# Performance work log

Measured on AMD Instinct MI355X. Metric: run time of the kernel, lower is better.

## Reference

```python
import jax, jax.numpy as jnp
import numpy as np

NEG = -1e30  # log-space -inf surrogate (safe for logaddexp in fp32)


def _ctc_mean_loss(y_true, y_pred):
    """tf.nn.ctc_loss with blank_index=-1, logit_length=T, label_length=#nonzero.

    y_true: [B, L] int labels, 0 = padding, packed at the front.
    y_pred: [B, T, C] logits. blank = C-1. Returns mean NLL over batch.
    """
    B, L = y_true.shape
    T, C = y_pred.shape[1], y_pred.shape[2]
    blank = C - 1
    S = 2 * L + 1  # extended label length (blanks interleaved)

    label_length = jnp.sum((y_true != 0).astype(jnp.int32), axis=1)  # [B]
    logp = jax.nn.log_softmax(y_pred, axis=-1)  # [B, T, C]

    # Extended sequence: blank, l1, blank, l2, ..., blank
    ext = jnp.full((B, S), blank, dtype=jnp.int32)
    ext = ext.at[:, 1::2].set(y_true.astype(jnp.int32))  # [B, S]

    # skip transition (s-2 -> s) allowed only at odd s>=3 when labels differ
    skip_ok = jnp.zeros((B, S), dtype=bool)
    skip_ok = skip_ok.at[:, 3::2].set(y_true[:, 1:] != y_true[:, :-1])

    # alpha_0
    alpha0 = jnp.full((B, S), NEG, dtype=logp.dtype)
    alpha0 = alpha0.at[:, 0].set(logp[:, 0, blank])
    alpha0 = alpha0.at[:, 1].set(
        jnp.take_along_axis(logp[:, 0, :], ext[:, 1:2], axis=1)[:, 0])

    def step(alpha, logp_t):  # alpha [B,S], logp_t [B,C]
        s1 = jnp.pad(alpha, ((0, 0), (1, 0)), constant_values=NEG)[:, :-1]
        s2 = jnp.pad(alpha, ((0, 0), (2, 0)), constant_values=NEG)[:, :-2]
        comb = jnp.logaddexp(jnp.logaddexp(alpha, s1),
                             jnp.where(skip_ok, s2, NEG))
        emit = jnp.take_along_axis(logp_t, ext, axis=1)  # [B,S]
        return comb + emit, None

    alphaT, _ = jax.lax.scan(step, alpha0, jnp.swapaxes(logp, 0, 1)[1:])

    # P(labels) = alpha_T[2l] + alpha_T[2l-1]  (last blank / last label)
    l = label_length
    idx = jnp.stack([2 * l, 2 * l - 1], axis=1)  # [B,2], l>=1 by construction
    fin = jnp.take_along_axis(alphaT, idx, axis=1)
    loss = -jnp.logaddexp(fin[:, 0], fin[:, 1])  # [B]
    return jnp.mean(loss)


def setup_inputs() -> dict:
    key = jax.random.key(0)
    k1, k2, k3 = jax.random.split(key, 3)
    B, T, L, C = 256, 512, 128, 128
    lengths = jax.random.randint(k1, (B,), L // 2, L + 1)  # labels per example
    vals = jax.random.randint(k2, (B, L), 1, C - 1)  # classes 1..C-2 (blank=C-1)
    mask = jnp.arange(L)[None, :] < lengths[:, None]
    y_true = jnp.where(mask, vals, 0).astype(jnp.int32)
    y_pred = jax.random.normal(k3, (B, T, C), dtype=jnp.float32)
    return {"y_true": y_true, "y_pred": y_pred}


def reference(y_true, y_pred):
    return _ctc_mean_loss(y_true, y_pred)
```

## Files before the change

### kernel.cpp

```cpp
#include <hip/hip_runtime.h>
#include <hip/hip_fp16.h>

#define LN2D 0.6931471805599453094172321

typedef float v2f __attribute__((ext_vector_type(2)));

__device__ __forceinline__ float shr1(float v, float fill) {
    return __int_as_float(__builtin_amdgcn_update_dpp(
        __float_as_int(fill), __float_as_int(v), 0x138 , 0xF, 0xF, false));
}
__device__ __forceinline__ float shl1(float v, float fill) {
    return __int_as_float(__builtin_amdgcn_update_dpp(
        __float_as_int(fill), __float_as_int(v), 0x130 , 0xF, 0xF, false));
}

__device__ __forceinline__ float wave_sum63(float x) {
    int t;
    t = __builtin_amdgcn_update_dpp(0, __float_as_int(x), 0x111, 0xF, 0xF, true);
    x += __int_as_float(t);
    t = __builtin_amdgcn_update_dpp(0, __float_as_int(x), 0x112, 0xF, 0xF, true);
    x += __int_as_float(t);
    t = __builtin_amdgcn_update_dpp(0, __float_as_int(x), 0x114, 0xF, 0xF, true);
    x += __int_as_float(t);
    t = __builtin_amdgcn_update_dpp(0, __float_as_int(x), 0x118, 0xF, 0xF, true);
    x += __int_as_float(t);
    t = __builtin_amdgcn_update_dpp(0, __float_as_int(x), 0x142, 0xA, 0xF, true);
    x += __int_as_float(t);
    t = __builtin_amdgcn_update_dpp(0, __float_as_int(x), 0x143, 0xC, 0xF, true);
    x += __int_as_float(t);
    return x;
}

__device__ __forceinline__ float wave_max63(float x) {
    int iv = __float_as_int(x); int t;
    t = __builtin_amdgcn_update_dpp(iv, iv, 0x111, 0xF, 0xF, false);
    x = fmaxf(x, __int_as_float(t)); iv = __float_as_int(x);
    t = __builtin_amdgcn_update_dpp(iv, iv, 0x112, 0xF, 0xF, false);
    x = fmaxf(x, __int_as_float(t)); iv = __float_as_int(x);
    t = __builtin_amdgcn_update_dpp(iv, iv, 0x114, 0xF, 0xF, false);
    x = fmaxf(x, __int_as_float(t)); iv = __float_as_int(x);
    t = __builtin_amdgcn_update_dpp(iv, iv, 0x118, 0xF, 0xF, false);
    x = fmaxf(x, __int_as_float(t)); iv = __float_as_int(x);
    t = __builtin_amdgcn_update_dpp(iv, iv, 0x142, 0xA, 0xF, false);
    x = fmaxf(x, __int_as_float(t)); iv = __float_as_int(x);
    t = __builtin_amdgcn_update_dpp(iv, iv, 0x143, 0xC, 0xF, false);
    x = fmaxf(x, __int_as_float(t));
    return x;
}

__device__ __forceinline__ float rdl63(float v) {
    return __int_as_float(__builtin_amdgcn_readlane(__float_as_int(v), 63));
}

__device__ __forceinline__ unsigned short pk_fp8(float a, float b) {
    const unsigned short ha = __builtin_bit_cast(unsigned short, __float2half_rn(a));
    const unsigned short hb = __builtin_bit_cast(unsigned short, __float2half_rn(b));
    const unsigned ua = ((unsigned)ha + 0x80u) >> 8;
    const unsigned ub = (((unsigned)hb + 0x80u) >> 8) << 8;
    return (unsigned short)(ua | ub);
}
__device__ __forceinline__ float dec_lo(unsigned short u) {
    return __half2float(__builtin_bit_cast(__half, (unsigned short)((u & 0xFFu) << 8)));
}
__device__ __forceinline__ float dec_hi(unsigned short u) {
    return __half2float(__builtin_bit_cast(__half, (unsigned short)(u & 0xFF00u)));
}

__global__ __launch_bounds__(512) void ctc_fused(const int* __restrict__ yt,
                                                 const float* __restrict__ yp,
                                                 float* __restrict__ part,
                                                 float* __restrict__ accW) {
    constexpr int L = 128;
    const int b    = blockIdx.x;
    const int w    = threadIdx.x >> 6;
    const int lane = threadIdx.x & 63;

    __shared__ unsigned short g[512][64];

    const int2 cc = *reinterpret_cast<const int2*>(yt + b * L + 2 * lane);
    const int c1 = cc.x, c3 = cc.y;
    const int sl1 = c1 >> 1, sh1v = (c1 & 1) << 4;
    const int sl3 = c3 >> 1, sh3v = (c3 & 1) << 4;

    float acc = 0.0f;
    const float* src = yp + ((size_t)b * 512 + w * 64) * 128 + lane * 2;
    v2f A8[8], B8[8];

#define ISSUE8(d_, p_)                                                         \
    asm volatile(                                                              \
        "global_load_dwordx2 %0, %8, off\n\t"                                  \
        "global_load_dwordx2 %1, %8, off offset:512\n\t"                       \
        "global_load_dwordx2 %2, %8, off offset:1024\n\t"                      \
        "global_load_dwordx2 %3, %8, off offset:1536\n\t"                      \
        "global_load_dwordx2 %4, %8, off offset:2048\n\t"                      \
        "global_load_dwordx2 %5, %8, off offset:2560\n\t"                      \
        "global_load_dwordx2 %6, %8, off offset:3072\n\t"                      \
        "global_load_dwordx2 %7, %8, off offset:3584"                          \
        : "=&v"(d_[0]), "=&v"(d_[1]), "=&v"(d_[2]), "=&v"(d_[3]),              \
          "=&v"(d_[4]), "=&v"(d_[5]), "=&v"(d_[6]), "=&v"(d_[7])               \
        : "v"(p_)                                                              \
        : "memory");

#define WAITN(n_)                                                              \
    {                                                                          \
        asm volatile("s_waitcnt vmcnt(" #n_ ")" ::: "memory");                 \
        __builtin_amdgcn_sched_barrier(0);                                     \
    }

#define PROC8(buf_, rb_)                                                       \
    {                                                                          \
        _Pragma("unroll")                                                      \
        for (int i = 0; i < 8; ++i) {                                          \
            const float vx = buf_[i].x, vy = buf_[i].y;                        \
            const float sall = rdl63(wave_sum63(__expf(vx) + __expf(vy)));     \
            const float xbv  = rdl63(vy);                \
            acc += __logf(sall) - xbv;                                         \
            const __half2 hh = __floats2half2_rn(vx, vy);                      \
            const int hb = __builtin_bit_cast(int, hh);                        \
            const int q1 = __shfl(hb, sl1, 64);                                \
            const int q3 = __shfl(hb, sl3, 64);                                \
            const float x1 = __half2float(__builtin_bit_cast(__half, (unsigned short)(q1 >> sh1v))); \
            const float x3 = __half2float(__builtin_bit_cast(__half, (unsigned short)(q3 >> sh3v))); \
            g[w * 64 + (rb_) + i][lane] = pk_fp8(__expf(x1 - xbv), __expf(x3 - xbv)); \
        }                                                                      \
    }

    ISSUE8(A8, src)
    ISSUE8(B8, src + 8 * 128)
    WAITN(8)  PROC8(A8, 0)   ISSUE8(A8, src + 16 * 128)
    WAITN(8)  PROC8(B8, 8)   ISSUE8(B8, src + 24 * 128)
    WAITN(8)  PROC8(A8, 16)  ISSUE8(A8, src + 32 * 128)
    WAITN(8)  PROC8(B8, 24)  ISSUE8(B8, src + 40 * 128)
    WAITN(8)  PROC8(A8, 32)  ISSUE8(A8, src + 48 * 128)
    WAITN(8)  PROC8(B8, 40)  ISSUE8(B8, src + 56 * 128)
    WAITN(8)  PROC8(A8, 48)
    WAITN(0)  PROC8(B8, 56)

    if (lane == 0) accW[b * 8 + w] = acc;
    __syncthreads();

    if (w == 0) {
        const int cprev = __shfl_up(c3, 1, 64);
        const float sk1 = (lane > 0 && c1 != cprev) ? 1.0f : 0.0f;
        const float sk3 = (c3 != c1) ? 1.0f : 0.0f;
        const float skB3 = shl1(sk1, 0.0f);
        const int llen = __popcll(__ballot(c1 != 0)) + __popcll(__ballot(c3 != 0));

        float o0, o1, o2, o3, o4;
        float q0, q1, q2, q3, q4;
        int   EF = 0, EB = 0;
        unsigned short fr[8], br[8];

#define RENORM5(a0_, a1_, a2_, a3_, a4_, Ec_)                                  \
    {                                                                          \
        float mr = fmaxf(fmaxf(fmaxf(a0_, a1_), fmaxf(a2_, a3_)), a4_);        \
        const float mru = rdl63(wave_max63(mr));                               \
        const int ie = (__float_as_int(mru) >> 23) & 0xFF;                     \
        const float sc = __int_as_float((253 - ie) << 23);                     \
        a0_ *= sc; a1_ *= sc; a2_ *= sc; a3_ *= sc; a4_ *= sc;                 \
        Ec_ += ie - 126;                                                       \
    }

#define FSTEP(bits_, rn_)                                                      \
    {                                                                          \
        const float e1 = dec_lo(bits_);                                        \
        const float e3 = dec_hi(bits_);                                        \
        const float pm = shr1(o3, 0.0f);                                       \
        const float n0 = o0 + pm;                                              \
        const float n1 = (o1 + o0 + sk1 * pm) * e1;                            \
        const float n2 = o2 + o1;                                              \
        const float n3 = (o3 + o2 + sk3 * o1) * e3;                            \
        o4 += o3;                                                              \
        o0 = n0; o1 = n1; o2 = n2; o3 = n3;                                    \
        if (rn_) RENORM5(o0, o1, o2, o3, o4, EF);                              \
    }

#define BSTEP(bits_, rn_)                                                      \
    {                                                                          \
        const float e1 = dec_lo(bits_);                                        \
        const float e3 = dec_hi(bits_);                                        \
        const float g1 = q1 * e1;                                              \
        const float g3 = q3 * e3;                                              \
        const float pm0 = shl1(q0, q4);          \
        const float pm1 = shl1(g1, 0.0f);        \
        const float n0 = q0 + g1;                                              \
        const float n1 = g1 + q2 + sk3 * g3;                                   \
        const float n2 = q2 + g3;                                              \
        const float n3 = g3 + pm0 + skB3 * pm1;                                \
        q0 = n0; q1 = n1; q2 = n2; q3 = n3;                                    \
        if (rn_) RENORM5(q0, q1, q2, q3, q4, EB);                              \
    }

        #pragma unroll
        for (int i = 0; i < 8; ++i) { fr[i] = g[i][lane]; br[i] = g[511 - i][lane]; }

        {
            const float e10 = dec_lo(fr[0]);
            o0 = (lane == 0) ? 1.0f : 0.0f;
            o1 = (lane == 0) ? e10 : 0.0f;
            o2 = 0.0f; o3 = 0.0f; o4 = 0.0f;
        }
        {
            const int sA = 2 * llen, sB = 2 * llen - 1;
            q0 = (4 * lane + 0 == sA) ? 1.0f : 0.0f;
            q1 = (4 * lane + 1 == sB) ? 1.0f : 0.0f;
            q2 = (4 * lane + 2 == sA) ? 1.0f : 0.0f;
            q3 = (4 * lane + 3 == sB) ? 1.0f : 0.0f;
            q4 = (llen == 128 && lane == 63) ? 1.0f : 0.0f;
        }

        BSTEP(br[0], false);
        fr[0] = g[8][lane]; br[0] = g[503][lane];
        #pragma unroll
        for (int k = 1; k < 8; ++k) {
            FSTEP(fr[k], false);
            BSTEP(br[k], false);
            fr[k] = g[k + 8][lane]; br[k] = g[511 - k - 8][lane];
        }
        for (int kb = 8; kb < 248; kb += 8) {
            #pragma unroll
            for (int j = 0; j < 8; ++j) {
                const int k = kb + j;
                FSTEP(fr[j], (k & 31) == 0);
                BSTEP(br[j], (k & 31) == 31);
                fr[j] = g[k + 8][lane]; br[j] = g[511 - k - 8][lane];
            }
        }
        #pragma unroll
        for (int k = 248; k < 256; ++k) {
            FSTEP(fr[k & 7], false);
            BSTEP(br[k & 7], (k & 31) == 31);
        }

        double p = (double)o0 * (double)q0 + (double)o1 * (double)q1
                 + (double)o2 * (double)q2 + (double)o3 * (double)q3;
        if (lane == 63) p += (double)o4 * (double)q4;
        #pragma unroll
        for (int off = 32; off > 0; off >>= 1) p += __shfl_xor(p, off, 64);
        if (lane == 0)
            part[b] = (float)(log(p) + (double)(EF + EB) * LN2D);
#undef BSTEP
#undef FSTEP
#undef RENORM5
    }
#undef PROC8
#undef WAITN
#undef ISSUE8
}

__global__ __launch_bounds__(256) void finalize(const float* __restrict__ part,
                                                const float* __restrict__ accW,
                                                float* __restrict__ out) {
    __shared__ float red[256];
    const int tid = threadIdx.x;
    float ls = 0.0f;
    #pragma unroll
    for (int j = 0; j < 8; ++j) ls += accW[tid * 8 + j];
    red[tid] = -(part[tid] - ls);
    __syncthreads();
    for (int off = 128; off > 0; off >>= 1) {
        if (tid < off) red[tid] += red[tid + off];
        __syncthreads();
    }
    if (tid == 0) out[0] = red[0] * (1.0f / 256.0f);
}

extern "C" void kernel_launch(void* const* d_in, const int* in_sizes, int n_in,
                              void* d_out, int out_size, void* d_ws, size_t ws_size,
                              hipStream_t stream) {
    constexpr int B = 256;
    const int*   y_true = (const int*)d_in[0];
    const float* y_pred = (const float*)d_in[1];
    float* out = (float*)d_out;

    float* part = (float*)d_ws;
    float* accW = part + B;

    ctc_fused<<<B, 512, 0, stream>>>(y_true, y_pred, part, accW);
    finalize<<<1, 256, 0, stream>>>(part, accW, out);
}
```

Measured before the change: 45.24 us.

## Compute log-sum-exp per lane over full rows and decode fp8 pairs in one op

The per-timestep softmax normaliser was computed with a wave-wide DPP reduction for every row. It is replaced by a second pass in which each lane reads one full 128-class row as float4 loads and sums exps serially. Only one wave reduction of the per-row logs remains per wave. The two-byte fp8-like decode is also merged into a single byte_perm plus half2-to-float2 conversion. The cost is re-reading the logits from global memory (likely L2-resident) in exchange for removing 64 cross-lane reductions per wave.

```diff
diff --git a/kernel.cpp b/kernel.cpp
--- a/kernel.cpp
+++ b/kernel.cpp
@@ -59,11 +59,9 @@
     const unsigned ub = (((unsigned)hb + 0x80u) >> 8) << 8;
     return (unsigned short)(ua | ub);
 }
-__device__ __forceinline__ float dec_lo(unsigned short u) {
-    return __half2float(__builtin_bit_cast(__half, (unsigned short)((u & 0xFFu) << 8)));
-}
-__device__ __forceinline__ float dec_hi(unsigned short u) {
-    return __half2float(__builtin_bit_cast(__half, (unsigned short)(u & 0xFF00u)));
+__device__ __forceinline__ float2 dec2(unsigned short u) {
+    const unsigned pk = __byte_perm((unsigned)u, 0u, 0x01040004);
+    return __half22float2(__builtin_bit_cast(__half2, pk));
 }
 
 __global__ __launch_bounds__(512) void ctc_fused(const int* __restrict__ yt,
@@ -82,7 +80,7 @@
     const int sl1 = c1 >> 1, sh1v = (c1 & 1) << 4;
     const int sl3 = c3 >> 1, sh3v = (c3 & 1) << 4;
 
-    float acc = 0.0f;
+    float xbsum = 0.0f;
     const float* src = yp + ((size_t)b * 512 + w * 64) * 128 + lane * 2;
     v2f A8[8], B8[8];
 
@@ -112,9 +110,8 @@
         _Pragma("unroll")                                                      \
         for (int i = 0; i < 8; ++i) {                                          \
             const float vx = buf_[i].x, vy = buf_[i].y;                        \
-            const float sall = rdl63(wave_sum63(__expf(vx) + __expf(vy)));     \
-            const float xbv  = rdl63(vy);                \
-            acc += __logf(sall) - xbv;                                         \
+            const float xbv = rdl63(vy);                 \
+            xbsum += xbv;                                                      \
             const __half2 hh = __floats2half2_rn(vx, vy);                      \
             const int hb = __builtin_bit_cast(int, hh);                        \
             const int q1 = __shfl(hb, sl1, 64);                                \
@@ -136,7 +133,18 @@
     WAITN(8)  PROC8(A8, 48)
     WAITN(0)  PROC8(B8, 56)
 
-    if (lane == 0) accW[b * 8 + w] = acc;
+    {
+        const float* pb = yp + ((size_t)b * 512 + w * 64 + lane) * 128;
+        float s = 0.0f;
+        #pragma unroll
+        for (int j = 0; j < 32; ++j) {
+            const float4 f = *reinterpret_cast<const float4*>(pb + 4 * j);
+            s += (__expf(f.x) + __expf(f.y)) + (__expf(f.z) + __expf(f.w));
+        }
+        const float lg = __logf(s);
+        const float tot = rdl63(wave_sum63(lg));
+        if (lane == 0) accW[b * 8 + w] = tot - xbsum;
+    }
     __syncthreads();
 
     if (w == 0) {
@@ -163,13 +171,12 @@
 
 #define FSTEP(bits_, rn_)                                                      \
     {                                                                          \
-        const float e1 = dec_lo(bits_);                                        \
-        const float e3 = dec_hi(bits_);                                        \
+        const float2 ee = dec2(bits_);                                         \
         const float pm = shr1(o3, 0.0f);                                       \
         const float n0 = o0 + pm;                                              \
-        const float n1 = (o1 + o0 + sk1 * pm) * e1;                            \
+        const float n1 = (o1 + o0 + sk1 * pm) * ee.x;                          \
         const float n2 = o2 + o1;                                              \
-        const float n3 = (o3 + o2 + sk3 * o1) * e3;                            \
+        const float n3 = (o3 + o2 + sk3 * o1) * ee.y;                          \
         o4 += o3;                                                              \
         o0 = n0; o1 = n1; o2 = n2; o3 = n3;                                    \
         if (rn_) RENORM5(o0, o1, o2, o3, o4, EF);                              \
@@ -177,10 +184,9 @@
 
 #define BSTEP(bits_, rn_)                                                      \
     {                                                                          \
-        const float e1 = dec_lo(bits_);                                        \
-        const float e3 = dec_hi(bits_);                                        \
-        const float g1 = q1 * e1;                                              \
-        const float g3 = q3 * e3;                                              \
+        const float2 ee = dec2(bits_);                                         \
+        const float g1 = q1 * ee.x;                                            \
+        const float g3 = q3 * ee.y;                                            \
         const float pm0 = shl1(q0, q4);          \
         const float pm1 = shl1(g1, 0.0f);        \
         const float n0 = q0 + g1;                                              \
@@ -195,9 +201,9 @@
         for (int i = 0; i < 8; ++i) { fr[i] = g[i][lane]; br[i] = g[511 - i][lane]; }
 
         {
-            const float e10 = dec_lo(fr[0]);
+            const float2 e0 = dec2(fr[0]);
             o0 = (lane == 0) ? 1.0f : 0.0f;
-            o1 = (lane == 0) ? e10 : 0.0f;
+            o1 = (lane == 0) ? e0.x : 0.0f;
             o2 = 0.0f; o3 = 0.0f; o4 = 0.0f;
         }
         {
```

Result: slower. 47.01 us (+3.9%).
